# Optimization experiments

Hardware: AMD Instinct MI355X
Metric: run time of the kernel (lower is better)

Reference implementation:

```python
import jax, jax.numpy as jnp
import numpy as np

H, W = 160, 160
FS = 7
SPAN = FS // 2
NUM_CLASSES = 19
NUM_ITERS = 5
THETA_ALPHA = 160.0  # scales rgb in bilateral features
THETA_BETA = 3.0     # scales position in bilateral features
THETA_GAMMA = 3.0    # scales position in spatial features
EPS = 1e-20

# offsets ordered (dx outer, dy inner) to match TF filter-tap index (dx+span)*FS + (dy+span)
OFFSETS = [(dx, dy) for dx in range(-SPAN, SPAN + 1) for dy in range(-SPAN, SPAN + 1)]


def _make_filter(features):
    # features: (bs, cf, H, W) -> gaussian affinity filter (bs, FS*FS, H, W)
    # filter[b, k, i, j] = exp(-0.5 * ||f[b,:,i+dx,j+dy] - f[b,:,i,j]||^2), 0 if out of bounds
    fp = jnp.pad(features, ((0, 0), (0, 0), (SPAN, SPAN), (SPAN, SPAN)))
    rows = jnp.arange(H)
    cols = jnp.arange(W)
    taps = []
    for dx, dy in OFFSETS:
        shifted = fp[:, :, SPAN + dx:SPAN + dx + H, SPAN + dy:SPAN + dy + W]
        aff = jnp.exp(-0.5 * jnp.sum((features - shifted) ** 2, axis=1))  # (bs, H, W)
        mask = (((rows + dx >= 0) & (rows + dx < H))[:, None]
                & ((cols + dy >= 0) & (cols + dy < W))[None, :])
        taps.append(aff * mask)
    return jnp.stack(taps, axis=1)  # (bs, FS*FS, H, W)


def _patches(x):
    # x: (bs, C, H, W) -> (bs, C, FS*FS, H, W), zero-padded shifts (matches extract_patches SAME)
    xp = jnp.pad(x, ((0, 0), (0, 0), (SPAN, SPAN), (SPAN, SPAN)))
    return jnp.stack(
        [xp[:, :, SPAN + dx:SPAN + dx + H, SPAN + dy:SPAN + dy + W] for dx, dy in OFFSETS],
        axis=2)


def _compute_gaussian(x, filt):
    # x: (bs, C, H, W), filt: (bs, FS*FS, H, W) -> (bs, C, H, W)
    return jnp.sum(_patches(x) * filt[:, None], axis=2)


def _forward(unaries, rgb, spatial_ker_weights, bilateral_ker_weights, compatibility_matrix):
    u = jnp.transpose(unaries, (0, 3, 1, 2))     # (bs, C, H, W)
    rgb_nchw = jnp.transpose(rgb, (0, 3, 1, 2))  # (bs, 3, H, W)
    bs = u.shape[0]
    mesh = jnp.stack(
        jnp.meshgrid(jnp.arange(H, dtype=jnp.float32), jnp.arange(W, dtype=jnp.float32),
                     indexing='ij'), 0)          # (2, H, W)
    spatial_feat = jnp.broadcast_to((mesh / THETA_GAMMA)[None], (bs, 2, H, W))
    bilateral_feat = jnp.concatenate(
        [rgb_nchw / THETA_ALPHA,
         jnp.broadcast_to((mesh / THETA_BETA)[None], (bs, 2, H, W))], axis=1)  # (bs, 5, H, W)

    spatial_filter = _make_filter(spatial_feat)
    bilateral_filter = _make_filter(bilateral_feat)

    ones = jnp.ones_like(u)
    spatial_norm = _compute_gaussian(ones, spatial_filter)
    bilateral_norm = _compute_gaussian(ones, bilateral_filter)

    q = u
    for _ in range(NUM_ITERS):
        # NOTE: original code does tf.nn.softmax(q_values, 0) -> softmax over the BATCH axis.
        sm = jax.nn.softmax(q, axis=0)
        s_out = _compute_gaussian(sm, spatial_filter) / (spatial_norm + EPS)
        b_out = _compute_gaussian(sm, bilateral_filter) / (bilateral_norm + EPS)
        msg = (jnp.einsum('kc,bchw->bkhw', spatial_ker_weights, s_out)
               + jnp.einsum('kc,bchw->bkhw', bilateral_ker_weights, b_out))
        pairwise = jnp.einsum('kc,bchw->bkhw', compatibility_matrix, msg)
        q = u - pairwise
    return jnp.transpose(q, (0, 2, 3, 1))  # (bs, H, W, C)


def setup_inputs() -> dict:
    key = jax.random.key(0)
    k1, k2 = jax.random.split(key)
    unaries = jax.random.normal(k1, (2, H, W, NUM_CLASSES), dtype=jnp.float32)
    rgb = jax.random.uniform(k2, (2, H, W, 3), dtype=jnp.float32) * 255.0
    eye = jnp.eye(NUM_CLASSES, dtype=jnp.float32)
    return {
        'unaries': unaries,
        'rgb': rgb,
        'spatial_ker_weights': eye,            # _diagonal_initializer
        'bilateral_ker_weights': eye,          # _diagonal_initializer
        'compatibility_matrix': -eye,          # _potts_model_initializer
    }


def reference(unaries, rgb, spatial_ker_weights, bilateral_ker_weights, compatibility_matrix):
    return _forward(unaries, rgb, spatial_ker_weights, bilateral_ker_weights,
                    compatibility_matrix)
```

## Files before the change

kernel.cpp:

```cpp
#include <hip/hip_runtime.h>


typedef __attribute__((ext_vector_type(4))) _Float16 half4;
typedef __attribute__((ext_vector_type(2))) _Float16 half2f;
typedef __attribute__((ext_vector_type(4))) float float4v;

#define HH 160
#define WW 160
#define NPIX (HH*WW)
#define NC 19
#define NG 5
#define SPAN 3
#define TR 8
#define TC 16
#define NPXT 128
#define LR 14
#define LC 22
#define LCP 24
#define HSTRIDE (LR*LCP)
#define NHALO (LR*LC)
#define NRING 180
#define NBLK 200
#define NTHR 640
#define EPSF 1e-20f
#define MAGICV 0x5EEDF00Du

#define BAR_CNT(k) (32 + (k)*32)

#define SZ_A    30720
#define OFF_WB  SZ_A
#define SHM_SZ  (SZ_A + 25*128*8)

__device__ __forceinline__ float fast_rcp(float x) { return __builtin_amdgcn_rcpf(x); }

__device__ __forceinline__ float smx0(float q0, float q1) {
    const float m  = fmaxf(q0, q1);
    const float e0 = __expf(q0 - m);
    const float e1 = __expf(q1 - m);
    return e0 * fast_rcp(e0 + e1);
}

__global__ void __launch_bounds__(NTHR) crf_kernel(
        const float* __restrict__ u,
        const float* __restrict__ rgb,
        const float* __restrict__ sw,
        const float* __restrict__ bw,
        const float* __restrict__ compat,
        unsigned long long* __restrict__ gsmA,
        unsigned long long* __restrict__ gsmB,
        unsigned* __restrict__ bar,
        float* __restrict__ out) {
    __shared__ __align__(16) char shm[SHM_SZ];
    __shared__ float Msh[960];
    __shared__ float rowsum[NC];
    __shared__ int   diagflag;
    float4*   rgbL = (float4*)shm;
    half4*    smH  = (half4*)shm;
    float*    accF = (float*)shm;
    unsigned* wbW  = (unsigned*)(shm + OFF_WB);
    const uint2* wbP = (const uint2*)(shm + OFF_WB);

    constexpr float WSPC[49] = {
        0.36787944f,0.48567179f,0.57375342f,0.60653066f,0.57375342f,0.48567179f,0.36787944f,
        0.48567179f,0.64118039f,0.75746513f,0.80073740f,0.75746513f,0.64118039f,0.48567179f,
        0.57375342f,0.75746513f,0.89483932f,0.94595947f,0.89483932f,0.75746513f,0.57375342f,
        0.60653066f,0.80073740f,0.94595947f,1.00000000f,0.94595947f,0.80073740f,0.60653066f,
        0.57375342f,0.75746513f,0.89483932f,0.94595947f,0.89483932f,0.75746513f,0.57375342f,
        0.48567179f,0.64118039f,0.75746513f,0.80073740f,0.75746513f,0.64118039f,0.48567179f,
        0.36787944f,0.48567179f,0.57375342f,0.60653066f,0.57375342f,0.48567179f,0.36787944f };

    const int tid = threadIdx.x;
    const int px  = tid & 127;
    const int g   = tid >> 7;
    const int r   = px >> 4, c = px & 15;
    const int ti0 = blockIdx.y * TR, tj0 = blockIdx.x * TC;
    const int gp  = (ti0 + r) * WW + (tj0 + c);
    const int ctr = (r + SPAN) * LCP + (c + SPAN);
    const int ku  = 4 * g;
    const int bid = blockIdx.y * 10 + blockIdx.x;

    if (bid == 0 && tid == 0) {
        #pragma unroll
        for (int k = 0; k < 8; ++k)
            __hip_atomic_store(&bar[BAR_CNT(k)], 0u, __ATOMIC_RELAXED, __HIP_MEMORY_SCOPE_AGENT);
        __hip_atomic_store(&bar[0], MAGICV, __ATOMIC_RELEASE, __HIP_MEMORY_SCOPE_AGENT);
    }
    if (tid == 0) {
        diagflag = 1;
        while (__hip_atomic_load(&bar[0], __ATOMIC_ACQUIRE, __HIP_MEMORY_SCOPE_AGENT) != MAGICV)
            __builtin_amdgcn_s_sleep(2);
    }
    if (tid < NC) {
        float rs = 0.0f;
        for (int cb = 0; cb < NC; ++cb) rs += sw[tid*NC + cb] + bw[tid*NC + cb];
        rowsum[tid] = rs;
    }
    __syncthreads();

    for (int e = tid; e < 960; e += NTHR) {
        const int k = e / 48, cc2 = e % 48;
        float acc = 0.0f;
        if (k < NC) {
            if (cc2 < NC) {
                for (int j = 0; j < NC; ++j) acc += compat[k*NC + j] * sw[j*NC + cc2];
            } else if (cc2 >= 20 && cc2 < 20 + NC) {
                const int cb = cc2 - 20;
                for (int j = 0; j < NC; ++j) acc += compat[k*NC + j] * bw[j*NC + cb];
            } else if (cc2 == 40) {
                for (int j = 0; j < NC; ++j) acc += compat[k*NC + j] * rowsum[j];
            }
        }
        Msh[e] = acc;
        bool off = false;
        if (k < NC) {
            if (cc2 < NC && cc2 != k && acc != 0.0f) off = true;
            if (cc2 >= 20 && cc2 < 20 + NC && (cc2 - 20) != k && acc != 0.0f) off = true;
        }
        if (off) atomicAnd(&diagflag, 0);
    }
    __syncthreads();

    float dsv[4], dbv[4];
    #pragma unroll
    for (int i = 0; i < 4; ++i) {
        dsv[i] = Msh[(ku + i) * 48 + (ku + i)];
        dbv[i] = Msh[(ku + i) * 48 + 20 + (ku + i)];
    }
    const bool isdiag = (diagflag != 0);

    for (int e = tid; e < 2 * NHALO; e += NTHR) {
        const int bb = e / NHALO, pos = e % NHALO;
        const int hr = pos / LC, hc = pos % LC;
        const int yi = ti0 - SPAN + hr, xj = tj0 - SPAN + hc;
        float4 rv = make_float4(0.f, 0.f, 0.f, 0.f);
        if ((unsigned)yi < HH && (unsigned)xj < WW) {
            const float* p = rgb + ((size_t)(bb * NPIX) + yi * WW + xj) * 3;
            rv = make_float4(p[0]*(1.f/160.f), p[1]*(1.f/160.f), p[2]*(1.f/160.f), 1.f);
        }
        rgbL[(bb ? HSTRIDE : 0) + hr * LCP + hc] = rv;
    }
    __syncthreads();

    {
        const float4 cv0 = rgbL[ctr];
        const float4 cv1 = rgbL[HSTRIDE + ctr];
        const int tapb = g * 10;
        const int ntap = (g == 4) ? 9 : 10;
        for (int i = 0; i < ntap; ++i) {
            const int t = tapb + i;
            const int dx = t / 7 - SPAN, dy = t % 7 - SPAN;
            const int n = ctr + dx * LCP + dy;
            const float4 nv0 = rgbL[n];
            const float4 nv1 = rgbL[HSTRIDE + n];
            const float wsm = __expf(-(float)(dx*dx + dy*dy) * (1.f/18.f)) * nv0.w;
            const float dr0 = cv0.x-nv0.x, dg0 = cv0.y-nv0.y, db0 = cv0.z-nv0.z;
            const float dr1 = cv1.x-nv1.x, dg1 = cv1.y-nv1.y, db1 = cv1.z-nv1.z;
            const float wb0 = wsm * __expf(-0.5f*(dr0*dr0+dg0*dg0+db0*db0));
            const float wb1 = wsm * __expf(-0.5f*(dr1*dr1+dg1*dg1+db1*db1));
            half2f hw = {(_Float16)wb0, (_Float16)wb1};
            unsigned uw; __builtin_memcpy(&uw, &hw, 4);
            wbW[(t >> 1) * 256 + px * 2 + (t & 1)] = uw;
        }
        if (g == 4) wbW[24 * 256 + px * 2 + 1] = 0u;
    }
    __syncthreads();

    float snI, bnI0, bnI1;
    {
        float sn = 0.f, bn0 = 0.f, bn1 = 0.f;
        #pragma unroll
        for (int t = 0; t < 49; ++t) {
            const unsigned uw = wbW[(t >> 1) * 256 + px * 2 + (t & 1)];
            half2f hw; __builtin_memcpy(&hw, &uw, 4);
            bn0 += (float)hw.x; bn1 += (float)hw.y;
            const int dx = t / 7 - SPAN, dy = t % 7 - SPAN;
            const int yi = ti0 + r + dx, xj = tj0 + c + dy;
            sn += (((unsigned)yi < HH) && ((unsigned)xj < WW)) ? WSPC[t] : 0.0f;
        }
        snI  = fast_rcp(sn + EPSF);
        bnI0 = fast_rcp(bn0 + EPSF);
        bnI1 = fast_rcp(bn1 + EPSF);
    }

    float uv0[4], uv1[4];
    #pragma unroll
    for (int i = 0; i < 4; ++i) {
        const int ch = 4*g + i;
        uv0[i] = (ch < NC) ? u[(size_t)gp * NC + ch] : 0.0f;
        uv1[i] = (ch < NC) ? u[((size_t)NPIX + gp) * NC + ch] : 0.0f;
    }
    half4 sh;
    #pragma unroll
    for (int i = 0; i < 4; ++i) sh[i] = (_Float16)smx0(uv0[i], uv1[i]);

    for (int it = 0; it < 5; ++it) {
        {
            unsigned long long u64; __builtin_memcpy(&u64, &sh, 8);
            unsigned long long* gdst = ((it & 1) ? gsmB : gsmA);
            __hip_atomic_store(&gdst[g * NPIX + gp], u64,
                               __ATOMIC_RELAXED, __HIP_MEMORY_SCOPE_AGENT);
        }
        __syncthreads();
        if (tid == 0) {
            __hip_atomic_fetch_add(&bar[BAR_CNT(bid & 7)], 1u,
                                   __ATOMIC_RELAXED, __HIP_MEMORY_SCOPE_AGENT);
            const unsigned tgt = (unsigned)(NBLK * (it + 1));
            unsigned sum;
            do {
                sum = 0;
                #pragma unroll
                for (int k = 0; k < 8; ++k)
                    sum += __hip_atomic_load(&bar[BAR_CNT(k)],
                                             __ATOMIC_RELAXED, __HIP_MEMORY_SCOPE_AGENT);
                if (sum < tgt) __builtin_amdgcn_s_sleep(2);
            } while (sum < tgt);
        }
        __syncthreads();

        const unsigned long long* gsrc = ((it & 1) ? gsmB : gsmA);
        smH[g * HSTRIDE + ctr] = sh;
        #pragma unroll
        for (int k2 = 0; k2 < 2; ++k2) {
            const int e = tid + NTHR * k2;
            if (e < NG * NRING) {
                const int sg = e / NRING, re = e - sg * NRING;
                int hr, hc;
                if (re < 66)        { hr = re / 22;          hc = re % 22; }
                else if (re < 132)  { const int t2 = re - 66;  hr = 11 + t2 / 22; hc = t2 % 22; }
                else                { const int t2 = re - 132; hr = 3 + t2 / 6;
                                      const int s = t2 % 6;    hc = (s < 3) ? s : s + 16; }
                const int yi = ti0 - SPAN + hr, xj = tj0 - SPAN + hc;
                half4 hv = (half4)(_Float16)0.0f;
                if ((unsigned)yi < HH && (unsigned)xj < WW) {
                    const unsigned long long raw =
                        __hip_atomic_load(&gsrc[sg * NPIX + yi * WW + xj],
                                          __ATOMIC_RELAXED, __HIP_MEMORY_SCOPE_AGENT);
                    __builtin_memcpy(&hv, &raw, 8);
                }
                smH[sg * HSTRIDE + hr * LCP + hc] = hv;
            }
        }
        __syncthreads();

        float4v sAv = (float4v)0.0f, b0a = (float4v)0.0f, b1a = (float4v)0.0f;
        const half4* pl = smH + g * HSTRIDE;
        #pragma unroll
        for (int i = 0; i < 24; ++i) {
            const uint2 wp = wbP[i * 128 + px];
            #pragma unroll
            for (int s = 0; s < 2; ++s) {
                const int t = 2*i + s;
                const int dx = t / 7 - SPAN, dy = t % 7 - SPAN;
                half2f hw; __builtin_memcpy(&hw, s ? &wp.y : &wp.x, 4);
                const float w0 = (float)hw.x, w1 = (float)hw.y;
                const half4 v = pl[ctr + dx*LCP + dy];
                const float4v f = {(float)v[0], (float)v[1], (float)v[2], (float)v[3]};
                sAv += WSPC[t] * f;
                b0a += w0 * f;
                b1a += w1 * f;
            }
        }
        {
            const uint2 wp = wbP[24 * 128 + px];
            half2f hw; __builtin_memcpy(&hw, &wp.x, 4);
            const float w0 = (float)hw.x, w1 = (float)hw.y;
            const half4 v = pl[ctr + SPAN*LCP + SPAN];
            const float4v f = {(float)v[0], (float)v[1], (float)v[2], (float)v[3]};
            sAv += WSPC[48] * f;
            b0a += w0 * f;
            b1a += w1 * f;
        }

        float q0v[4], q1v[4];
        if (isdiag) {
            #pragma unroll
            for (int i = 0; i < 4; ++i) {
                const float sAn = sAv[i] * snI;
                const float b0n = b0a[i] * bnI0;
                const float b1x = b1a[i] * bnI1;
                q0v[i] = uv0[i] - dsv[i]*sAn - dbv[i]*b0n;
                q1v[i] = uv1[i] - (dsv[i] + dbv[i]) + dsv[i]*sAn + dbv[i]*b1x;
            }
        } else {
            __syncthreads();
            #pragma unroll
            for (int i = 0; i < 4; ++i) {
                accF[(4*g + i) * NPXT + px]      = sAv[i] * snI;
                accF[(20 + 4*g + i) * NPXT + px] = b0a[i] * bnI0;
                accF[(40 + 4*g + i) * NPXT + px] = b1a[i] * bnI1;
            }
            __syncthreads();
            float t1[4] = {0,0,0,0}, t2[4] = {0,0,0,0}, t3[4] = {0,0,0,0};
            #pragma unroll
            for (int cc = 0; cc < 20; ++cc) {
                const float sv  = accF[cc * NPXT + px];
                const float b0v = accF[(20 + cc) * NPXT + px];
                const float b1v = accF[(40 + cc) * NPXT + px];
                #pragma unroll
                for (int i = 0; i < 4; ++i) {
                    const float* mk = Msh + (ku + i) * 48;
                    t1[i] += mk[cc] * sv;
                    t2[i] += mk[20 + cc] * b0v;
                    t3[i] += mk[20 + cc] * b1v;
                }
            }
            #pragma unroll
            for (int i = 0; i < 4; ++i) {
                const float rs = Msh[(ku + i) * 48 + 40];
                q0v[i] = uv0[i] - t1[i] - t2[i];
                q1v[i] = uv1[i] - rs + t1[i] + t3[i];
            }
        }

        if (it == 4) {
            #pragma unroll
            for (int i = 0; i < 4; ++i) {
                const int ch = 4*g + i;
                if (ch < NC) {
                    out[(size_t)gp * NC + ch]          = q0v[i];
                    out[((size_t)NPIX + gp) * NC + ch] = q1v[i];
                }
            }
        } else {
            #pragma unroll
            for (int i = 0; i < 4; ++i) sh[i] = (_Float16)smx0(q0v[i], q1v[i]);
        }
    }
}

extern "C" void kernel_launch(void* const* d_in, const int* in_sizes, int n_in,
                              void* d_out, int out_size, void* d_ws, size_t ws_size,
                              hipStream_t stream) {
    const float* u      = (const float*)d_in[0];
    const float* rgb    = (const float*)d_in[1];
    const float* sw     = (const float*)d_in[2];
    const float* bw     = (const float*)d_in[3];
    const float* compat = (const float*)d_in[4];
    float* out = (float*)d_out;

    unsigned long long* gsmA = (unsigned long long*)d_ws;
    unsigned long long* gsmB = (unsigned long long*)((char*)d_ws + 1024000);
    unsigned* bar = (unsigned*)((char*)d_ws + 2048000);

    crf_kernel<<<dim3(WW/TC, HH/TR, 1), dim3(NTHR), 0, stream>>>(
        u, rgb, sw, bw, compat, gsmA, gsmB, bar, out);
}
```

Baseline: 111.5 us.

## Replace grid-wide barrier with neighbor-only epoch flags between iterations

```diff
diff --git a/kernel.cpp b/kernel.cpp
--- a/kernel.cpp
+++ b/kernel.cpp
@@ -25,7 +25,7 @@
 #define EPSF 1e-20f
 #define MAGICV 0x5EEDF00Du
 
-#define BAR_CNT(k) (32 + (k)*32)
+#define EPW(b) (32 + (b)*32)
 
 #define SZ_A    30720
 #define OFF_WB  SZ_A
@@ -79,11 +79,26 @@
     const int ku  = 4 * g;
     const int bid = blockIdx.y * 10 + blockIdx.x;
 
-    if (bid == 0 && tid == 0) {
+    int nb[8];
+    {
+        const int bx = blockIdx.x, by = blockIdx.y;
+        int k = 0;
         #pragma unroll
-        for (int k = 0; k < 8; ++k)
-            __hip_atomic_store(&bar[BAR_CNT(k)], 0u, __ATOMIC_RELAXED, __HIP_MEMORY_SCOPE_AGENT);
-        __hip_atomic_store(&bar[0], MAGICV, __ATOMIC_RELEASE, __HIP_MEMORY_SCOPE_AGENT);
+        for (int dy2 = -1; dy2 <= 1; ++dy2)
+            #pragma unroll
+            for (int dx2 = -1; dx2 <= 1; ++dx2) {
+                if (dx2 == 0 && dy2 == 0) continue;
+                const int nx = bx + dx2, ny = by + dy2;
+                nb[k++] = ((unsigned)nx < 10u && (unsigned)ny < 20u) ? (ny*10 + nx) : bid;
+            }
+    }
+
+    if (bid == 0) {
+        for (int e = tid; e < NBLK; e += NTHR)
+            __hip_atomic_store(&bar[EPW(e)], 0u, __ATOMIC_RELAXED, __HIP_MEMORY_SCOPE_AGENT);
+        __syncthreads();
+        if (tid == 0)
+            __hip_atomic_store(&bar[0], MAGICV, __ATOMIC_RELEASE, __HIP_MEMORY_SCOPE_AGENT);
     }
     if (tid == 0) {
         diagflag = 1;
@@ -202,18 +217,20 @@
         }
         __syncthreads();
         if (tid == 0) {
-            __hip_atomic_fetch_add(&bar[BAR_CNT(bid & 7)], 1u,
-                                   __ATOMIC_RELAXED, __HIP_MEMORY_SCOPE_AGENT);
-            const unsigned tgt = (unsigned)(NBLK * (it + 1));
-            unsigned sum;
+            __hip_atomic_store(&bar[EPW(bid)], (unsigned)(it + 1),
+                               __ATOMIC_RELAXED, __HIP_MEMORY_SCOPE_AGENT);
+            const unsigned tgt = (unsigned)(it + 1);
+            unsigned mn;
             do {
-                sum = 0;
+                mn = 0xFFFFFFFFu;
                 #pragma unroll
-                for (int k = 0; k < 8; ++k)
-                    sum += __hip_atomic_load(&bar[BAR_CNT(k)],
-                                             __ATOMIC_RELAXED, __HIP_MEMORY_SCOPE_AGENT);
-                if (sum < tgt) __builtin_amdgcn_s_sleep(2);
-            } while (sum < tgt);
+                for (int k = 0; k < 8; ++k) {
+                    const unsigned e = __hip_atomic_load(&bar[EPW(nb[k])],
+                                                         __ATOMIC_RELAXED, __HIP_MEMORY_SCOPE_AGENT);
+                    mn = (e < mn) ? e : mn;
+                }
+                if (mn < tgt) __builtin_amdgcn_s_sleep(1);
+            } while (mn < tgt);
         }
         __syncthreads();
 
```

Measured after the change: 108.4 us. -2.7%, faster.
